# Kernel optimization log

Measured on AMD Instinct MI355X. Metric: run time of the kernel, lower is better.

The kernel has to match this reference:

```python
import jax, jax.numpy as jnp
import numpy as np

GDEP = 3
ALPHA = 0.05
C_IN = 32
C_OUT = 32


def setup_inputs() -> dict:
    key = jax.random.key(0)
    k1, k2, k3, k4 = jax.random.split(key, 4)
    B, C, V, L = 16, C_IN, 512, 168
    x = jax.random.normal(k1, (B, C, V, L), dtype=jnp.float32)
    adj = jax.random.uniform(k2, (V, V), dtype=jnp.float32)
    fan_in = (GDEP + 1) * C_IN  # Conv2d 1x1: kaiming-uniform-ish init
    bound = 1.0 / np.sqrt(fan_in)
    W = jax.random.uniform(k3, (C_OUT, fan_in), minval=-bound, maxval=bound, dtype=jnp.float32)
    b = jax.random.uniform(k4, (C_OUT,), minval=-bound, maxval=bound, dtype=jnp.float32)
    return {"x": x, "adj": adj, "W": W, "b": b}


def reference(x, adj, W, b):
    V = adj.shape[0]
    a = adj + jnp.eye(V, dtype=adj.dtype)
    d = a.sum(axis=1)
    a = a / d[:, None]                      # row-normalized adjacency [V, V]
    h = x
    outs = [h]
    for _ in range(GDEP):                   # small fixed depth loop
        prop = jnp.einsum('ncvl,vw->ncwl', h, a)
        h = ALPHA * x + (1.0 - ALPHA) * prop
        outs.append(h)
    ho = jnp.concatenate(outs, axis=1)      # [B, (gdep+1)*C, V, L]
    # 1x1 conv == channel contraction
    out = jnp.einsum('bcvl,oc->bovl', ho, W) + b[None, :, None, None]
    return out
```

## Files before the change

kernel.cpp:

```cpp
#include <hip/hip_runtime.h>

#define V 512
#define L 168
#define PLANE 86016
#define CHSTRIDE 2752512
#define B_ 16
#define HDR4 (1u << 22)

typedef __attribute__((ext_vector_type(8))) short s16x8;
typedef __attribute__((ext_vector_type(4))) float f32x4;
typedef unsigned short u16;

__device__ inline short f2bf(float f) {
    unsigned u = __builtin_bit_cast(unsigned, f);
    u += 0x7FFF + ((u >> 16) & 1);
    return (short)(u >> 16);
}
__device__ inline float bf2f(u16 s) {
    return __builtin_bit_cast(float, ((unsigned)s) << 16);
}
__device__ inline void gll16(const u16* g, u16* lds) {
    __builtin_amdgcn_global_load_lds(
        (const __attribute__((address_space(1))) void*)g,
        (__attribute__((address_space(3))) void*)lds, 16, 0, 0);
}

__global__ __launch_bounds__(256) void prep2(const float* __restrict__ adj,
                                             const float* __restrict__ W,
                                             u16* __restrict__ M1,
                                             u16* __restrict__ ANb,
                                             u16* __restrict__ Wb) {
    if (blockIdx.x == V) {
        const float al = 0.05f, be = 0.95f;
        for (int i = threadIdx.x; i < 1024; i += 256) {
            const int o = i >> 5, c = i & 31;
            const float w0 = W[o * 128 + c];
            const float w1 = W[o * 128 + 32 + c];
            const float w2 = W[o * 128 + 64 + c];
            const float w3 = W[o * 128 + 96 + c];
            Wb[o * 128 + c]      = f2bf(w0 + al * (w1 + w2 + w3));
            Wb[o * 128 + 32 + c] = f2bf(be * (w1 + al * (w2 + w3)));
            Wb[o * 128 + 64 + c] = f2bf(be * be * (w2 + al * w3));
            Wb[o * 128 + 96 + c] = f2bf(be * be * be * w3);
        }
        return;
    }
    const int v = blockIdx.x;
    float s = 0.f;
    for (int w = threadIdx.x; w < V; w += 256)
        s += adj[v * V + w] + (w == v ? 1.f : 0.f);
    __shared__ float red[256];
    red[threadIdx.x] = s;
    __syncthreads();
    for (int off = 128; off > 0; off >>= 1) {
        if ((int)threadIdx.x < off) red[threadIdx.x] += red[threadIdx.x + off];
        __syncthreads();
    }
    const float inv = 1.f / red[0];
    for (int w = threadIdx.x; w < V; w += 256) {
        const short q = f2bf((adj[v * V + w] + (w == v ? 1.f : 0.f)) * inv);
        M1[w * V + v] = q;
        ANb[v * V + w] = q;
    }
}

__global__ __launch_bounds__(256) void powk(const u16* __restrict__ X,
                                            const u16* __restrict__ ANb,
                                            u16* __restrict__ OUT) {
    const int w0 = (blockIdx.x >> 3) * 64, v0 = (blockIdx.x & 7) * 64;
    const int tid = threadIdx.x, lane = tid & 63, wave = tid >> 6;
    const int colb = lane & 15, kg = lane >> 4;
    f32x4 acc[4];
#pragma unroll
    for (int i = 0; i < 4; i++) acc[i] = (f32x4){0.f, 0.f, 0.f, 0.f};
#pragma unroll 4
    for (int kk = 0; kk < 16; kk++) {
        const int u = kk * 32 + kg * 8;
        const s16x8 bfr = *(const s16x8*)&ANb[(size_t)(v0 + wave * 16 + colb) * 512 + u];
#pragma unroll
        for (int mt = 0; mt < 4; mt++) {
            const s16x8 afr = *(const s16x8*)&X[(size_t)(w0 + mt * 16 + colb) * 512 + u];
            acc[mt] = __builtin_amdgcn_mfma_f32_16x16x32_bf16(afr, bfr, acc[mt], 0, 0, 0);
        }
    }
#pragma unroll
    for (int mt = 0; mt < 4; mt++)
#pragma unroll
        for (int r = 0; r < 4; r++)
            OUT[(size_t)(w0 + mt * 16 + kg * 4 + r) * 512 + v0 + wave * 16 + colb] =
                (u16)f2bf(acc[mt][r]);
}

__global__ __launch_bounds__(256) void cvtT(const float* __restrict__ x,
                                            u16* __restrict__ xa) {
    const int b = blockIdx.z >> 5, c = blockIdx.z & 31;
    const int v0 = blockIdx.y * 64, l0 = blockIdx.x * 64;
    const int tid = threadIdx.x;
    __shared__ float T[64][65];
    const float* xp = x + (size_t)b * CHSTRIDE + (size_t)c * PLANE;
    u16* xo = xa + (size_t)b * CHSTRIDE;
#pragma unroll
    for (int rep = 0; rep < 16; rep++) {
        const int idx = rep * 256 + tid;
        const int vv = idx >> 6, ll = idx & 63;
        if (l0 + ll < L) T[vv][ll] = xp[(size_t)(v0 + vv) * L + l0 + ll];
    }
    __syncthreads();
#pragma unroll
    for (int rep = 0; rep < 16; rep++) {
        const int idx = rep * 256 + tid;
        const int ll = idx >> 6, vv = idx & 63;
        if (l0 + ll < L)
            xo[(size_t)((l0 + ll) * 32 + c) * 512 + v0 + vv] = f2bf(T[vv][ll]);
    }
}

__global__ __launch_bounds__(256, 2) void propOut2(const u16* __restrict__ xa,
                                                   const u16* __restrict__ AS,
                                                   const u16* __restrict__ Wb,
                                                   const float* __restrict__ bias,
                                                   u16* __restrict__ tmpb) {
    const int b = blockIdx.z;
    const int logical = (blockIdx.x & 7) * 21 + (blockIdx.x >> 3);
    const int ntile = logical >> 2, wq = logical & 3;
    const int n0 = ntile * 128, w0 = wq * 128, l0 = ntile * 4;
    const int tid = threadIdx.x, lane = tid & 63, wave = tid >> 6;
    const int wm = wave >> 1, wn = wave & 1;
    const int colb = lane & 15, kg = lane >> 4;
    __shared__ __align__(16) u16 SHf[32768];
    const size_t sB = (size_t)b * CHSTRIDE;
    const u16* srcb = xa + sB;

    f32x4 acc1[4][4], acc2[4][4], acc3[4][4];
#pragma unroll
    for (int i = 0; i < 4; i++)
#pragma unroll
        for (int j = 0; j < 4; j++) {
            acc1[i][j] = (f32x4){0.f, 0.f, 0.f, 0.f};
            acc2[i][j] = acc1[i][j];
            acc3[i][j] = acc1[i][j];
        }

    const u16* gsrc = (wave == 3) ? srcb + (size_t)n0 * 512
                                  : AS + (size_t)wave * 262144 + (size_t)w0 * 512;
    u16* ldst = &SHf[wave * 8192];

    for (int t = 0; t < 8; ++t) {
        __syncthreads();
#pragma unroll
        for (int oh = 0; oh < 16; ++oh) {
            const int oct = oh >> 1, h = oh & 1;
            gll16(gsrc + (size_t)(h * 64 + lane) * 512 + t * 64 + oct * 8,
                  ldst + oct * 1024 + h * 512 + lane * 8);
        }
        __syncthreads();
        __builtin_amdgcn_s_setprio(1);
#pragma unroll
        for (int kk = 0; kk < 2; ++kk) {
            const int cq = kk * 4 + kg;
            s16x8 bfr[4];
#pragma unroll
            for (int nt = 0; nt < 4; nt++)
                bfr[nt] = *(const s16x8*)&SHf[24576 + cq * 1024 +
                                              (wn * 64 + nt * 16 + colb) * 8];
#pragma unroll
            for (int mt = 0; mt < 4; mt++) {
                const int aoff = cq * 1024 + (wm * 64 + mt * 16 + colb) * 8;
                const s16x8 a1 = *(const s16x8*)&SHf[aoff];
                const s16x8 a2 = *(const s16x8*)&SHf[8192 + aoff];
                const s16x8 a3 = *(const s16x8*)&SHf[16384 + aoff];
#pragma unroll
                for (int nt = 0; nt < 4; nt++) {
                    acc1[mt][nt] = __builtin_amdgcn_mfma_f32_16x16x32_bf16(a1, bfr[nt],
                                                                           acc1[mt][nt], 0, 0, 0);
                    acc2[mt][nt] = __builtin_amdgcn_mfma_f32_16x16x32_bf16(a2, bfr[nt],
                                                                           acc2[mt][nt], 0, 0, 0);
                    acc3[mt][nt] = __builtin_amdgcn_mfma_f32_16x16x32_bf16(a3, bfr[nt],
                                                                           acc3[mt][nt], 0, 0, 0);
                }
            }
        }
        __builtin_amdgcn_s_setprio(0);
    }

#define BOUNCE(ACC)                                                               \
    _Pragma("unroll") for (int mt = 0; mt < 4; mt++) {                            \
        const int wr = wm * 64 + mt * 16 + kg * 4;                                \
        _Pragma("unroll") for (int nt = 0; nt < 4; nt++) {                        \
            const int nn = wn * 64 + nt * 16 + colb;                              \
            _Pragma("unroll") for (int r = 0; r < 4; r++)                         \
                SHf[(wr + r) * 136 + nn] = (u16)f2bf(ACC[mt][nt][r]);             \
        }                                                                         \
    }

#define OUTACC(KP)                                                                \
    _Pragma("unroll") for (int pf = 0; pf < 8; pf++) {                            \
        const s16x8 bfr = *(const s16x8*)&SHf[(pf * 16 + colb) * 136 +            \
                                              wave * 32 + kg * 8];                \
        _Pragma("unroll") for (int mt = 0; mt < 2; mt++) {                        \
            const s16x8 afr = *(const s16x8*)&Wb[(mt * 16 + colb) * 128 +         \
                                                 (KP) * 32 + kg * 8];             \
            aco[mt][pf] = __builtin_amdgcn_mfma_f32_16x16x32_bf16(                \
                afr, bfr, aco[mt][pf], 0, 0, 0);                                  \
        }                                                                         \
    }

    __syncthreads();
    BOUNCE(acc1);
    __syncthreads();

    f32x4 aco[2][8];
#pragma unroll
    for (int i = 0; i < 2; i++)
#pragma unroll
        for (int j = 0; j < 8; j++) aco[i][j] = (f32x4){0.f, 0.f, 0.f, 0.f};

#pragma unroll
    for (int pf = 0; pf < 8; pf++) {
        s16x8 bfr;
#pragma unroll
        for (int j = 0; j < 8; j++)
            bfr[j] = (short)srcb[(size_t)(n0 + wave * 32 + kg * 8 + j) * 512 +
                                 w0 + pf * 16 + colb];
#pragma unroll
        for (int mt = 0; mt < 2; mt++) {
            const s16x8 afr = *(const s16x8*)&Wb[(mt * 16 + colb) * 128 + kg * 8];
            aco[mt][pf] = __builtin_amdgcn_mfma_f32_16x16x32_bf16(afr, bfr, aco[mt][pf], 0, 0, 0);
        }
    }
    OUTACC(1);
    __syncthreads();
    BOUNCE(acc2);
    __syncthreads();
    OUTACC(2);
    __syncthreads();
    BOUNCE(acc3);
    __syncthreads();
    OUTACC(3);
#undef BOUNCE
#undef OUTACC

#pragma unroll
    for (int mt = 0; mt < 2; mt++)
#pragma unroll
        for (int pf = 0; pf < 8; pf++)
#pragma unroll
            for (int r = 0; r < 4; r++) {
                const int o = mt * 16 + kg * 4 + r;
                tmpb[sB + (size_t)o * PLANE + (size_t)(l0 + wave) * 512 +
                     w0 + pf * 16 + colb] = (u16)f2bf(bias[o] + aco[mt][pf][r]);
            }
}

__global__ __launch_bounds__(256) void transT_b(const u16* __restrict__ tmpb,
                                                float* __restrict__ out) {
    const int o = blockIdx.y, b = blockIdx.z;
    const int vt = blockIdx.x / 3, lt = blockIdx.x % 3;
    const int v0 = vt * 64, l0 = lt * 64;
    const int tid = threadIdx.x;
    __shared__ float T[64][65];
    const u16* tp = tmpb + (size_t)b * CHSTRIDE + (size_t)o * PLANE;
    float* op = out + (size_t)b * CHSTRIDE + (size_t)o * PLANE;
#pragma unroll
    for (int rep = 0; rep < 16; rep++) {
        const int idx = rep * 256 + tid;
        const int ll = idx >> 6, vv = idx & 63;
        if (l0 + ll < L) T[ll][vv] = bf2f(tp[(size_t)(l0 + ll) * 512 + v0 + vv]);
    }
    __syncthreads();
#pragma unroll
    for (int rep = 0; rep < 16; rep++) {
        const int idx = rep * 256 + tid;
        const int vv = idx >> 6, ll = idx & 63;
        if (l0 + ll < L) op[(size_t)(v0 + vv) * L + l0 + ll] = T[ll][vv];
    }
}

extern "C" void kernel_launch(void* const* d_in, const int* in_sizes, int n_in,
                              void* d_out, int out_size, void* d_ws, size_t ws_size,
                              hipStream_t stream) {
    const float* x = (const float*)d_in[0];
    const float* adj = (const float*)d_in[1];
    const float* W = (const float*)d_in[2];
    const float* bias = (const float*)d_in[3];
    float* out = (float*)d_out;

    u16* AS = (u16*)d_ws;
    u16* M1 = AS;
    u16* M2 = AS + 262144;
    u16* M3 = AS + 2 * 262144;
    u16* ANb = AS + 3 * 262144;
    u16* Wb = AS + 4 * 262144;
    u16* hbuf = (u16*)((char*)d_ws + HDR4);

    prep2<<<V + 1, 256, 0, stream>>>(adj, W, M1, ANb, Wb);
    powk<<<64, 256, 0, stream>>>(M1, ANb, M2);
    powk<<<64, 256, 0, stream>>>(M2, ANb, M3);

    const size_t avail = ws_size > HDR4 ? ws_size - HDR4 : 0;
    int nbc = (int)(avail / ((size_t)4 * CHSTRIDE));
    if (nbc < 1) nbc = 1;
    if (nbc > B_) nbc = B_;

    for (int b0 = 0; b0 < B_; b0 += nbc) {
        const int nb = (B_ - b0 < nbc) ? (B_ - b0) : nbc;
        const float* xb = x + (size_t)b0 * CHSTRIDE;
        float* outb = out + (size_t)b0 * CHSTRIDE;
        u16* xa = hbuf;
        u16* tmpb = hbuf + (size_t)nbc * CHSTRIDE;

        cvtT<<<dim3(3, 8, nb * 32), 256, 0, stream>>>(xb, xa);
        propOut2<<<dim3(168, 1, nb), 256, 0, stream>>>(xa, AS, Wb, bias, tmpb);
        transT_b<<<dim3(24, 32, nb), 256, 0, stream>>>(tmpb, outb);
    }
}
```

Baseline: 515.8 us.

## Double-buffer LDS staging in propOut and move adjacency scratch into output tail

The propagation GEMM loop now uses two LDS buffers with a K-step of 32. The global-to-LDS load for the next step is issued before the MFMAs for the current step, so each iteration needs one barrier instead of two. The precomputed adjacency powers and bf16 weights now sit in the tail of the output buffer rather than the start of the workspace. That frees the whole workspace for batch chunks and may mean fewer chunk launches. This relies on the last chunk's transpose writing the tail only after propOut has finished reading the matrices, and the shorter K-steps add loop overhead.

New measurement: 500.6 us. -2.9%, faster.

```diff
diff --git a/kernel.cpp b/kernel.cpp
--- a/kernel.cpp
+++ b/kernel.cpp
@@ -5,7 +5,7 @@
 #define PLANE 86016
 #define CHSTRIDE 2752512
 #define B_ 16
-#define HDR4 (1u << 22)
+#define HDRE 1052672
 
 typedef __attribute__((ext_vector_type(8))) short s16x8;
 typedef __attribute__((ext_vector_type(4))) float f32x4;
@@ -115,11 +115,11 @@
     }
 }
 
-__global__ __launch_bounds__(256, 2) void propOut2(const u16* __restrict__ xa,
-                                                   const u16* __restrict__ AS,
-                                                   const u16* __restrict__ Wb,
-                                                   const float* __restrict__ bias,
-                                                   u16* __restrict__ tmpb) {
+__global__ __launch_bounds__(256, 2) void propOut(const u16* __restrict__ xa,
+                                                  const u16* __restrict__ AS,
+                                                  const u16* __restrict__ Wb,
+                                                  const float* __restrict__ bias,
+                                                  u16* __restrict__ tmpb) {
     const int b = blockIdx.z;
     const int logical = (blockIdx.x & 7) * 21 + (blockIdx.x >> 3);
     const int ntile = logical >> 2, wq = logical & 3;
@@ -127,9 +127,13 @@
     const int tid = threadIdx.x, lane = tid & 63, wave = tid >> 6;
     const int wm = wave >> 1, wn = wave & 1;
     const int colb = lane & 15, kg = lane >> 4;
-    __shared__ __align__(16) u16 SHf[32768];
+    __shared__ __align__(16) u16 SH[2][16384];
+    u16* flat = &SH[0][0];
     const size_t sB = (size_t)b * CHSTRIDE;
     const u16* srcb = xa + sB;
+
+    const u16* gsrc = (wave == 3) ? srcb + (size_t)n0 * 512
+                                  : AS + (size_t)wave * 262144 + (size_t)w0 * 512;
 
     f32x4 acc1[4][4], acc2[4][4], acc3[4][4];
 #pragma unroll
@@ -141,47 +145,52 @@
             acc3[i][j] = acc1[i][j];
         }
 
-    const u16* gsrc = (wave == 3) ? srcb + (size_t)n0 * 512
-                                  : AS + (size_t)wave * 262144 + (size_t)w0 * 512;
-    u16* ldst = &SHf[wave * 8192];
-
-    for (int t = 0; t < 8; ++t) {
+#define STAGE(T, BUF)                                                             \
+    {                                                                             \
+        const int v0s = (T) * 32;                                                 \
+        _Pragma("unroll") for (int i = 0; i < 8; i++) {                           \
+            const int oct = i >> 1, half = i & 1;                                 \
+            const int row = half * 64 + lane;                                     \
+            gll16(gsrc + (size_t)row * 512 + v0s + oct * 8,                       \
+                  &SH[BUF][wave * 4096 + oct * 1024 + half * 512]);               \
+        }                                                                         \
+    }
+
+#define MFMASTEP(BUF)                                                             \
+    {                                                                             \
+        s16x8 bfr[4];                                                             \
+        _Pragma("unroll") for (int nt = 0; nt < 4; nt++)                          \
+            bfr[nt] = *(const s16x8*)&SH[BUF][12288 + kg * 1024 +                 \
+                                             (wn * 64 + nt * 16 + colb) * 8];     \
+        _Pragma("unroll") for (int mt = 0; mt < 4; mt++) {                        \
+            const int aoff = kg * 1024 + (wm * 64 + mt * 16 + colb) * 8;          \
+            const s16x8 a1 = *(const s16x8*)&SH[BUF][aoff];                       \
+            const s16x8 a2 = *(const s16x8*)&SH[BUF][4096 + aoff];                \
+            const s16x8 a3 = *(const s16x8*)&SH[BUF][8192 + aoff];                \
+            _Pragma("unroll") for (int nt = 0; nt < 4; nt++) {                    \
+                acc1[mt][nt] = __builtin_amdgcn_mfma_f32_16x16x32_bf16(           \
+                    a1, bfr[nt], acc1[mt][nt], 0, 0, 0);                          \
+                acc2[mt][nt] = __builtin_amdgcn_mfma_f32_16x16x32_bf16(           \
+                    a2, bfr[nt], acc2[mt][nt], 0, 0, 0);                          \
+                acc3[mt][nt] = __builtin_amdgcn_mfma_f32_16x16x32_bf16(           \
+                    a3, bfr[nt], acc3[mt][nt], 0, 0, 0);                          \
+            }                                                                     \
+        }                                                                         \
+    }
+
+    STAGE(0, 0);
+    __syncthreads();
+#pragma unroll
+    for (int t = 0; t < 16; t++) {
+        const int buf = t & 1;
+        if (t < 15) STAGE(t + 1, buf ^ 1);
+        __builtin_amdgcn_s_setprio(1);
+        MFMASTEP(buf);
+        __builtin_amdgcn_s_setprio(0);
         __syncthreads();
-#pragma unroll
-        for (int oh = 0; oh < 16; ++oh) {
-            const int oct = oh >> 1, h = oh & 1;
-            gll16(gsrc + (size_t)(h * 64 + lane) * 512 + t * 64 + oct * 8,
-                  ldst + oct * 1024 + h * 512 + lane * 8);
-        }
-        __syncthreads();
-        __builtin_amdgcn_s_setprio(1);
-#pragma unroll
-        for (int kk = 0; kk < 2; ++kk) {
-            const int cq = kk * 4 + kg;
-            s16x8 bfr[4];
-#pragma unroll
-            for (int nt = 0; nt < 4; nt++)
-                bfr[nt] = *(const s16x8*)&SHf[24576 + cq * 1024 +
-                                              (wn * 64 + nt * 16 + colb) * 8];
-#pragma unroll
-            for (int mt = 0; mt < 4; mt++) {
-                const int aoff = cq * 1024 + (wm * 64 + mt * 16 + colb) * 8;
-                const s16x8 a1 = *(const s16x8*)&SHf[aoff];
-                const s16x8 a2 = *(const s16x8*)&SHf[8192 + aoff];
-                const s16x8 a3 = *(const s16x8*)&SHf[16384 + aoff];
-#pragma unroll
-                for (int nt = 0; nt < 4; nt++) {
-                    acc1[mt][nt] = __builtin_amdgcn_mfma_f32_16x16x32_bf16(a1, bfr[nt],
-                                                                           acc1[mt][nt], 0, 0, 0);
-                    acc2[mt][nt] = __builtin_amdgcn_mfma_f32_16x16x32_bf16(a2, bfr[nt],
-                                                                           acc2[mt][nt], 0, 0, 0);
-                    acc3[mt][nt] = __builtin_amdgcn_mfma_f32_16x16x32_bf16(a3, bfr[nt],
-                                                                           acc3[mt][nt], 0, 0, 0);
-                }
-            }
-        }
-        __builtin_amdgcn_s_setprio(0);
-    }
+    }
+#undef MFMASTEP
+#undef STAGE
 
 #define BOUNCE(ACC)                                                               \
     _Pragma("unroll") for (int mt = 0; mt < 4; mt++) {                            \
@@ -189,14 +198,14 @@
         _Pragma("unroll") for (int nt = 0; nt < 4; nt++) {                        \
             const int nn = wn * 64 + nt * 16 + colb;                              \
             _Pragma("unroll") for (int r = 0; r < 4; r++)                         \
-                SHf[(wr + r) * 136 + nn] = (u16)f2bf(ACC[mt][nt][r]);             \
+                flat[(wr + r) * 136 + nn] = (u16)f2bf(ACC[mt][nt][r]);            \
         }                                                                         \
     }
 
 #define OUTACC(KP)                                                                \
     _Pragma("unroll") for (int pf = 0; pf < 8; pf++) {                            \
-        const s16x8 bfr = *(const s16x8*)&SHf[(pf * 16 + colb) * 136 +            \
-                                              wave * 32 + kg * 8];                \
+        const s16x8 bfr = *(const s16x8*)&flat[(pf * 16 + colb) * 136 +           \
+                                               wave * 32 + kg * 8];               \
         _Pragma("unroll") for (int mt = 0; mt < 2; mt++) {                        \
             const s16x8 afr = *(const s16x8*)&Wb[(mt * 16 + colb) * 128 +         \
                                                  (KP) * 32 + kg * 8];             \
@@ -205,7 +214,6 @@
         }                                                                         \
     }
 
-    __syncthreads();
     BOUNCE(acc1);
     __syncthreads();
 
@@ -285,20 +293,20 @@
     const float* bias = (const float*)d_in[3];
     float* out = (float*)d_out;
 
-    u16* AS = (u16*)d_ws;
+    u16* hdr = (u16*)((char*)d_out + (size_t)out_size * 4 - (size_t)HDRE * 2 - 256);
+    u16* AS = hdr;
     u16* M1 = AS;
     u16* M2 = AS + 262144;
     u16* M3 = AS + 2 * 262144;
     u16* ANb = AS + 3 * 262144;
     u16* Wb = AS + 4 * 262144;
-    u16* hbuf = (u16*)((char*)d_ws + HDR4);
+    u16* hbuf = (u16*)d_ws;
 
     prep2<<<V + 1, 256, 0, stream>>>(adj, W, M1, ANb, Wb);
     powk<<<64, 256, 0, stream>>>(M1, ANb, M2);
     powk<<<64, 256, 0, stream>>>(M2, ANb, M3);
 
-    const size_t avail = ws_size > HDR4 ? ws_size - HDR4 : 0;
-    int nbc = (int)(avail / ((size_t)4 * CHSTRIDE));
+    int nbc = (int)(ws_size / ((size_t)4 * CHSTRIDE));
     if (nbc < 1) nbc = 1;
     if (nbc > B_) nbc = B_;
 
@@ -310,7 +318,7 @@
         u16* tmpb = hbuf + (size_t)nbc * CHSTRIDE;
 
         cvtT<<<dim3(3, 8, nb * 32), 256, 0, stream>>>(xb, xa);
-        propOut2<<<dim3(168, 1, nb), 256, 0, stream>>>(xa, AS, Wb, bias, tmpb);
+        propOut<<<dim3(168, 1, nb), 256, 0, stream>>>(xa, AS, Wb, bias, tmpb);
         transT_b<<<dim3(24, 32, nb), 256, 0, stream>>>(tmpb, outb);
     }
 }
```
